# Optimization experiments

Measured on AMD Instinct MI355X. Metric: run time of the kernel, lower is better.

Reference implementation:

```python
import jax, jax.numpy as jnp
import numpy as np

N = 50000
IN_F = 200
OUT_F = 200
NRELA = 200
E1 = 400000
E2 = 100000
ALPHA = 0.2  # leakyrelu slope


def setup_inputs() -> dict:
    key = jax.random.key(0)
    ks = jax.random.split(key, 9)
    xav = float(np.sqrt(2.0 / (OUT_F + 2 * IN_F + NRELA))) * 1.414
    return {
        "x": jax.random.normal(ks[0], (N, IN_F), dtype=jnp.float32),
        "edge": jax.random.randint(ks[1], (2, E1), 0, N, dtype=jnp.int32),
        "edge_embed": jax.random.normal(ks[2], (E1, NRELA), dtype=jnp.float32),
        "edge_list_nhop": jax.random.randint(ks[3], (2, E2), 0, N, dtype=jnp.int32),
        "edge_embed_nhop": jax.random.normal(ks[4], (E2, NRELA), dtype=jnp.float32),
        "a": jax.random.normal(ks[5], (OUT_F, 2 * IN_F + NRELA), dtype=jnp.float32) * xav,
        "a_2": jax.random.normal(ks[6], (1, OUT_F), dtype=jnp.float32) * float(np.sqrt(2.0 / (1 + OUT_F))) * 1.414,
        "mlp_w": jax.random.normal(ks[7], (1, OUT_F), dtype=jnp.float32) * float(np.sqrt(1.0 / OUT_F)),
        "mlp_b": jnp.zeros((1,), dtype=jnp.float32),
    }


def reference(x, edge, edge_embed, edge_list_nhop, edge_embed_nhop, a, a_2, mlp_w, mlp_b):
    # concat 1-hop and n-hop edges: e [2,E], emb [E,nrela]
    e = jnp.concatenate([edge, edge_list_nhop], axis=1)
    emb = jnp.concatenate([edge_embed, edge_embed_nhop], axis=0)
    src = e[0]
    dst = e[1]
    n_edges = emb.shape[0]
    # edge_h: [E, 2*in + nrela]
    edge_h = jnp.concatenate([x[src], x[dst], emb], axis=1)
    # edge_m = a @ edge_h.T, kept as [E, out]
    edge_m = edge_h @ a.T
    # powers = -leakyrelu(a_2 @ edge_m): [E]
    powers = -jax.nn.leaky_relu(edge_m @ a_2[0], ALPHA)
    # inline MLP: tanh(Linear(edge_m)) -> [E]
    y = jnp.tanh(edge_m @ mlp_w[0] + mlp_b[0])
    powers = powers * y / n_edges
    edge_e = jnp.exp(powers)  # [E]
    n = x.shape[0]
    # segment-sum over source nodes (sparse.sum over dim=1 of coo[src,dst,:])
    e_rowsum = jax.ops.segment_sum(edge_e, src, num_segments=n)[:, None]  # [N,1]
    e_rowsum = jnp.where(e_rowsum == 0.0, 1e-12, e_rowsum)
    # weighted scatter-add of edge messages
    edge_w = edge_e[:, None] * edge_m  # [E, out]
    h_prime = jax.ops.segment_sum(edge_w, src, num_segments=n)  # [N, out]
    h_prime = h_prime / e_rowsum
    return jax.nn.elu(h_prime)  # concat=True
```

## Files before the change

### kernel.cpp

```cpp
#include <hip/hip_runtime.h>
#include <math.h>

#define NN    50000
#define FDIM  200
#define E1N   400000
#define E2N   100000
#define EN    500000

typedef __attribute__((ext_vector_type(8))) short short8;
typedef __attribute__((ext_vector_type(4))) float f32x4;

#define VALL_OFF   0
#define WALL_OFF   608
#define SCAL_OFF   1216
#define RS_OFF     201216
#define CNT_OFF    251216
#define FILL_OFF   301216
#define INCL_OFF   351216
#define BSUM_OFF   401216
#define SORT_OFF   401472
#define XB_OFF     1401472
#define AB_OFF     6401472
#define TSB_OFF    6461472

static __device__ __forceinline__ unsigned short f2bf(float f) {
    unsigned int u = __float_as_uint(f);
    unsigned int r = (u + 0x7fffu + ((u >> 16) & 1u)) >> 16;
    return (unsigned short)r;
}
static __device__ __forceinline__ float bf2f(unsigned short s) {
    return __uint_as_float((unsigned int)s << 16);
}

#define DPP_ADD(x, ctrl, rmask) \
    x += __int_as_float(__builtin_amdgcn_update_dpp(0, __float_as_int(x), ctrl, rmask, 0xf, true))

static __device__ __forceinline__ float wave_sum_bcast(float x) {
    DPP_ADD(x, 0x111, 0xf);
    DPP_ADD(x, 0x112, 0xf);
    DPP_ADD(x, 0x114, 0xf);
    DPP_ADD(x, 0x118, 0xf);
    DPP_ADD(x, 0x142, 0xa);
    DPP_ADD(x, 0x143, 0xc);
    return __int_as_float(__builtin_amdgcn_readlane(__float_as_int(x), 63));
}

__global__ void k_coeffs(const float* __restrict__ a, const float* __restrict__ a2,
                         const float* __restrict__ mlpw,
                         float* __restrict__ vall, float* __restrict__ wall) {
    int k = blockIdx.x * blockDim.x + threadIdx.x;
    if (k >= 600) return;
    float v = 0.f, w = 0.f;
    for (int o = 0; o < FDIM; ++o) {
        float av = a[o * 600 + k];
        v += a2[o] * av;
        w += mlpw[o] * av;
    }
    vall[k] = v;
    wall[k] = w;
}

__global__ __launch_bounds__(256) void k_node_scal(const float* __restrict__ x,
                                                   const float* __restrict__ vall,
                                                   const float* __restrict__ wall,
                                                   float* __restrict__ scal,
                                                   unsigned short* __restrict__ xb) {
    __shared__ float sv[1200];
    int tid = threadIdx.x;
    for (int i = tid; i < 1200; i += 256) sv[i] = (i < 600) ? vall[i] : wall[i - 600];
    __syncthreads();
    int lane = tid & 63;
    int n = blockIdx.x * 4 + (tid >> 6);
    float ps = 0.f, pd = 0.f, qs = 0.f, qd = 0.f;
    if (lane < 50) {
        float4 xv = *(const float4*)(x + (size_t)n * FDIM + lane * 4);
        float4 v1 = *(const float4*)(sv + lane * 4);
        float4 v2 = *(const float4*)(sv + 200 + lane * 4);
        float4 w1 = *(const float4*)(sv + 600 + lane * 4);
        float4 w2 = *(const float4*)(sv + 800 + lane * 4);
        ps = xv.x * v1.x + xv.y * v1.y + xv.z * v1.z + xv.w * v1.w;
        pd = xv.x * v2.x + xv.y * v2.y + xv.z * v2.z + xv.w * v2.w;
        qs = xv.x * w1.x + xv.y * w1.y + xv.z * w1.z + xv.w * w1.w;
        qd = xv.x * w2.x + xv.y * w2.y + xv.z * w2.z + xv.w * w2.w;
        ushort4 o;
        o.x = f2bf(xv.x); o.y = f2bf(xv.y); o.z = f2bf(xv.z); o.w = f2bf(xv.w);
        *(ushort4*)(xb + (size_t)n * FDIM + lane * 4) = o;
    }
    ps = wave_sum_bcast(ps);
    pd = wave_sum_bcast(pd);
    qs = wave_sum_bcast(qs);
    qd = wave_sum_bcast(qd);
    if (lane == 0) {
        float4 r = make_float4(ps, pd, qs, qd);
        *(float4*)(scal + (size_t)n * 4) = r;
    }
}

__global__ __launch_bounds__(256) void k_cvt(const float* __restrict__ src,
                                             unsigned short* __restrict__ dst, int n4) {
    int i = blockIdx.x * 256 + threadIdx.x;
    if (i >= n4) return;
    float4 v = *(const float4*)(src + (size_t)i * 4);
    ushort4 o;
    o.x = f2bf(v.x); o.y = f2bf(v.y); o.z = f2bf(v.z); o.w = f2bf(v.w);
    *(ushort4*)(dst + (size_t)i * 4) = o;
}

__global__ __launch_bounds__(256) void k_hist(const int* __restrict__ edge,
                                              const int* __restrict__ edgenh,
                                              int* __restrict__ counts) {
    int g = blockIdx.x * 256 + threadIdx.x;
    if (g >= EN) return;
    int s = (g < E1N) ? edge[g] : edgenh[g - E1N];
    atomicAdd(counts + s, 1);
}

__global__ __launch_bounds__(256) void k_scan1(const int* __restrict__ counts,
                                               int* __restrict__ incl,
                                               int* __restrict__ bsums) {
    __shared__ int tmp[256];
    int g = blockIdx.x * 256 + threadIdx.x;
    int v = (g < NN) ? counts[g] : 0;
    tmp[threadIdx.x] = v;
    __syncthreads();
    for (int off = 1; off < 256; off <<= 1) {
        int t = (threadIdx.x >= off) ? tmp[threadIdx.x - off] : 0;
        __syncthreads();
        tmp[threadIdx.x] += t;
        __syncthreads();
    }
    if (g < NN) incl[g] = tmp[threadIdx.x];
    if (threadIdx.x == 255) bsums[blockIdx.x] = tmp[255];
}

__global__ __launch_bounds__(256) void k_scan2(int* __restrict__ bsums, int nb) {
    __shared__ int tmp[256];
    int v = (threadIdx.x < nb) ? bsums[threadIdx.x] : 0;
    tmp[threadIdx.x] = v;
    __syncthreads();
    for (int off = 1; off < 256; off <<= 1) {
        int t = (threadIdx.x >= off) ? tmp[threadIdx.x - off] : 0;
        __syncthreads();
        tmp[threadIdx.x] += t;
        __syncthreads();
    }
    if (threadIdx.x < nb) bsums[threadIdx.x] = tmp[threadIdx.x] - v;
}

__global__ __launch_bounds__(256) void k_scan3(const int* __restrict__ counts,
                                               int* __restrict__ incl,
                                               const int* __restrict__ bsums,
                                               int* __restrict__ fill) {
    int g = blockIdx.x * 256 + threadIdx.x;
    if (g >= NN) return;
    int v = incl[g] - counts[g] + bsums[blockIdx.x];
    incl[g] = v;
    fill[g] = v;
}

__global__ __launch_bounds__(256) void k_scatter(const int* __restrict__ edge,
                                                 const int* __restrict__ edgenh,
                                                 int* __restrict__ fill,
                                                 int2* __restrict__ sorted2) {
    int g = blockIdx.x * 256 + threadIdx.x;
    if (g >= EN) return;
    int s, d;
    if (g < E1N) { s = edge[g]; d = edge[E1N + g]; }
    else { s = edgenh[g - E1N]; d = edgenh[E2N + (g - E1N)]; }
    int pos = atomicAdd(fill + s, 1);
    sorted2[pos] = make_int2(g, d);
}

__global__ __launch_bounds__(256) void k_csr(const int2* __restrict__ sorted2,
                                             const int* __restrict__ offs,
                                             const int* __restrict__ counts,
                                             const float* __restrict__ ee,
                                             const float* __restrict__ eenh,
                                             const unsigned short* __restrict__ xb,
                                             const float* __restrict__ vall,
                                             const float* __restrict__ wall,
                                             const float* __restrict__ scal,
                                             const float* __restrict__ mlpb,
                                             float* __restrict__ rowsum,
                                             unsigned short* __restrict__ Tsb) {
    int tid = threadIdx.x, lane = tid & 63;
    int n = blockIdx.x * 4 + (tid >> 6);
    float4 v3 = make_float4(0, 0, 0, 0), w3 = v3;
    if (lane < 50) {
        v3 = *(const float4*)(vall + 400 + lane * 4);
        w3 = *(const float4*)(wall + 400 + lane * 4);
    }
    float4 sc_n = *(const float4*)(scal + (size_t)n * 4);
    float mb = mlpb[0];
    int beg = offs[n], cnt = counts[n];
    float accx0 = 0, accx1 = 0, accx2 = 0, accx3 = 0;
    float acce0 = 0, acce1 = 0, acce2 = 0, acce3 = 0;
    float rs = 0.f;
    int2 ed = (cnt > 0) ? sorted2[beg] : make_int2(0, 0);
    float4 evc = make_float4(0, 0, 0, 0), xvc = evc;
    if (cnt > 0 && lane < 50) {
        const float* er = (ed.x < E1N) ? ee + (size_t)ed.x * FDIM
                                       : eenh + (size_t)(ed.x - E1N) * FDIM;
        evc = *(const float4*)(er + lane * 4);
        ushort4 xu = *(const ushort4*)(xb + (size_t)ed.y * FDIM + lane * 4);
        xvc.x = bf2f(xu.x); xvc.y = bf2f(xu.y); xvc.z = bf2f(xu.z); xvc.w = bf2f(xu.w);
    }
    for (int i = 0; i < cnt; ++i) {
        int2 edn = (i + 1 < cnt) ? sorted2[beg + i + 1] : ed;
        float4 evn = make_float4(0, 0, 0, 0), xvn = evn;
        if (i + 1 < cnt && lane < 50) {
            const float* ern = (edn.x < E1N) ? ee + (size_t)edn.x * FDIM
                                             : eenh + (size_t)(edn.x - E1N) * FDIM;
            evn = *(const float4*)(ern + lane * 4);
            ushort4 xu = *(const ushort4*)(xb + (size_t)edn.y * FDIM + lane * 4);
            xvn.x = bf2f(xu.x); xvn.y = bf2f(xu.y); xvn.z = bf2f(xu.z); xvn.w = bf2f(xu.w);
        }
        float pe = evc.x * v3.x + evc.y * v3.y + evc.z * v3.z + evc.w * v3.w;
        float qe = evc.x * w3.x + evc.y * w3.y + evc.z * w3.z + evc.w * w3.w;
        pe = wave_sum_bcast(pe);
        qe = wave_sum_bcast(qe);
        float4 sd = *(const float4*)(scal + (size_t)ed.y * 4);
        float z1 = sc_n.x + sd.y + pe;
        float z2 = sc_n.z + sd.w + qe + mb;
        float l = z1 > 0.f ? z1 : 0.2f * z1;
        float e2 = __expf(2.f * z2);
        float t = 1.f - 2.f * __builtin_amdgcn_rcpf(e2 + 1.f);
        float wgt = __expf(l * t * (-1.f / (float)EN));
        rs += wgt;
        accx0 += wgt * xvc.x; accx1 += wgt * xvc.y; accx2 += wgt * xvc.z; accx3 += wgt * xvc.w;
        acce0 += wgt * evc.x; acce1 += wgt * evc.y; acce2 += wgt * evc.z; acce3 += wgt * evc.w;
        ed = edn; evc = evn; xvc = xvn;
    }
    if (lane == 0) rowsum[n] = rs;
    float inv = (cnt > 0) ? __builtin_amdgcn_rcpf(rs) : 0.f;
    if (lane < 50) {
        ushort4 o1, o2;
        o1.x = f2bf(accx0 * inv); o1.y = f2bf(accx1 * inv);
        o1.z = f2bf(accx2 * inv); o1.w = f2bf(accx3 * inv);
        o2.x = f2bf(acce0 * inv); o2.y = f2bf(acce1 * inv);
        o2.z = f2bf(acce2 * inv); o2.w = f2bf(acce3 * inv);
        *(ushort4*)(Tsb + (size_t)n * 400 + lane * 4) = o1;
        *(ushort4*)(Tsb + (size_t)n * 400 + 200 + lane * 4) = o2;
    }
}

__global__ __launch_bounds__(256) void k_gemm_fused(const unsigned short* __restrict__ xb,
                                                    const unsigned short* __restrict__ tsb,
                                                    const unsigned short* __restrict__ ab,
                                                    const float* __restrict__ rowsum,
                                                    float* __restrict__ out) {
    __shared__ unsigned short Al[64][40];
    __shared__ unsigned short Bl[64][40];
    int tid = threadIdx.x, w = tid >> 6, lane = tid & 63;
    int h = blockIdx.y * 4 + blockIdx.x;
    int g = (h & 7) * 391 + (h >> 3);
    int by = g >> 2, bx = g & 3;
    f32x4 acc[4] = {};
    int r = tid >> 2, c = tid & 3;
    int arow = by * 64 + r;
    int brow = bx * 64 + r;
    bool inA = arow < NN;
    bool inB = brow < 200;
    const unsigned short* aPx = xb + (size_t)arow * 200;
    const unsigned short* aPt = tsb + (size_t)arow * 400;
    const unsigned short* bP = ab + (size_t)brow * 600;
    for (int k0 = 0; k0 < 640; k0 += 32) {
        int gk = k0 + c * 8;
        uint4 av = make_uint4(0, 0, 0, 0), bv = av;
        if (gk < 200) {
            if (inA) av = *(const uint4*)(aPx + gk);
            if (inB) bv = *(const uint4*)(bP + gk);
        } else if (gk >= 224 && gk < 624) {
            if (inA) av = *(const uint4*)(aPt + (gk - 224));
            if (inB) bv = *(const uint4*)(bP + gk - 24);
        }
        *(uint4*)&Al[r][c * 8] = av;
        *(uint4*)&Bl[r][c * 8] = bv;
        __syncthreads();
        short8 af = *(short8*)&Al[w * 16 + (lane & 15)][(lane >> 4) * 8];
        #pragma unroll
        for (int ct = 0; ct < 4; ++ct) {
            short8 bf = *(short8*)&Bl[ct * 16 + (lane & 15)][(lane >> 4) * 8];
            acc[ct] = __builtin_amdgcn_mfma_f32_16x16x32_bf16(af, bf, acc[ct], 0, 0, 0);
        }
        __syncthreads();
    }
    #pragma unroll
    for (int ct = 0; ct < 4; ++ct) {
        #pragma unroll
        for (int rr = 0; rr < 4; ++rr) {
            int grow = by * 64 + w * 16 + (lane >> 4) * 4 + rr;
            int gcol = bx * 64 + ct * 16 + (lane & 15);
            if (grow < NN && gcol < 200) {
                float rsv = rowsum[grow];
                float hh = acc[ct][rr];
                float o = (rsv == 0.f) ? 0.f : (hh > 0.f ? hh : expm1f(hh));
                out[(size_t)grow * 200 + gcol] = o;
            }
        }
    }
}

extern "C" void kernel_launch(void* const* d_in, const int* in_sizes, int n_in,
                              void* d_out, int out_size, void* d_ws, size_t ws_size,
                              hipStream_t stream) {
    const float* x      = (const float*)d_in[0];
    const int*   edge   = (const int*)d_in[1];
    const float* ee     = (const float*)d_in[2];
    const int*   edgenh = (const int*)d_in[3];
    const float* eenh   = (const float*)d_in[4];
    const float* a      = (const float*)d_in[5];
    const float* a2     = (const float*)d_in[6];
    const float* mlpw   = (const float*)d_in[7];
    const float* mlpb   = (const float*)d_in[8];

    float* ws = (float*)d_ws;
    float* vall   = ws + VALL_OFF;
    float* wall   = ws + WALL_OFF;
    float* scal   = ws + SCAL_OFF;
    float* rowsum = ws + RS_OFF;
    int*   counts = (int*)(ws + CNT_OFF);
    int*   fill   = (int*)(ws + FILL_OFF);
    int*   incl   = (int*)(ws + INCL_OFF);
    int*   bsums  = (int*)(ws + BSUM_OFF);
    int2*  sorted2 = (int2*)(ws + SORT_OFF);
    unsigned short* xb  = (unsigned short*)(ws + XB_OFF);
    unsigned short* ab  = (unsigned short*)(ws + AB_OFF);
    unsigned short* tsb = (unsigned short*)(ws + TSB_OFF);

    hipMemsetAsync(counts, 0, (size_t)(2 * NN) * sizeof(int), stream);

    k_coeffs<<<3, 256, 0, stream>>>(a, a2, mlpw, vall, wall);
    k_node_scal<<<NN / 4, 256, 0, stream>>>(x, vall, wall, scal, xb);
    k_cvt<<<(200 * 600 / 4 + 255) / 256, 256, 0, stream>>>(a, ab, 200 * 600 / 4);

    k_hist<<<(EN + 255) / 256, 256, 0, stream>>>(edge, edgenh, counts);
    int nb = (NN + 255) / 256;
    k_scan1<<<nb, 256, 0, stream>>>(counts, incl, bsums);
    k_scan2<<<1, 256, 0, stream>>>(bsums, nb);
    k_scan3<<<nb, 256, 0, stream>>>(counts, incl, bsums, fill);
    k_scatter<<<(EN + 255) / 256, 256, 0, stream>>>(edge, edgenh, fill, sorted2);

    k_csr<<<NN / 4, 256, 0, stream>>>(sorted2, incl, counts, ee, eenh, xb,
                                      vall, wall, scal, mlpb, rowsum, tsb);

    dim3 gg(4, (NN + 63) / 64);
    k_gemm_fused<<<gg, 256, 0, stream>>>(xb, tsb, ab, rowsum, (float*)d_out);
}
```

Before: 727.6 us.

## Batch edge records per wave and prefetch four gathers ahead in CSR loop

The per-node edge loop now loads up to 64 edge records, plus the destination node's scalar terms, in one coalesced per-lane read and broadcasts them with readlane. This replaces the serial sorted2 and scal loads that sat on each iteration's critical path. Gathers of edge-embedding and x rows are kept four edges in flight with a rotating set of registers, instead of one edge ahead. The costs are higher register pressure, padding to a multiple of four with masked-out weights, and readlane of zeroed records, which issues gathers of row 0 for padded slots.

```diff
diff --git a/kernel.cpp b/kernel.cpp
--- a/kernel.cpp
+++ b/kernel.cpp
@@ -43,6 +43,10 @@
     DPP_ADD(x, 0x142, 0xa);
     DPP_ADD(x, 0x143, 0xc);
     return __int_as_float(__builtin_amdgcn_readlane(__float_as_int(x), 63));
+}
+
+static __device__ __forceinline__ float readlane_f(float v, int l) {
+    return __int_as_float(__builtin_amdgcn_readlane(__float_as_int(v), l));
 }
 
 __global__ void k_coeffs(const float* __restrict__ a, const float* __restrict__ a2,
@@ -171,6 +175,37 @@
     sorted2[pos] = make_int2(g, d);
 }
 
+#define ISSUE(EV, XU, IDX) do {                                                   \
+    int _e = __builtin_amdgcn_readlane(recx, (IDX));                              \
+    int _d = __builtin_amdgcn_readlane(recy, (IDX));                              \
+    const float* _er = (_e < E1N) ? ee + (size_t)_e * FDIM                        \
+                                  : eenh + (size_t)(_e - E1N) * FDIM;             \
+    if (lane < 50) {                                                              \
+        EV = *(const float4*)(_er + lane * 4);                                    \
+        XU = *(const ushort4*)(xb + (size_t)_d * FDIM + lane * 4);                \
+    }                                                                             \
+} while (0)
+
+#define CONSUME(EV, XU, IDX) do {                                                 \
+    float _pe = EV.x * v3.x + EV.y * v3.y + EV.z * v3.z + EV.w * v3.w;            \
+    float _qe = EV.x * w3.x + EV.y * w3.y + EV.z * w3.z + EV.w * w3.w;            \
+    _pe = wave_sum_bcast(_pe);                                                    \
+    _qe = wave_sum_bcast(_qe);                                                    \
+    float _sdy = readlane_f(sdy, (IDX));                                          \
+    float _sdw = readlane_f(sdw, (IDX));                                          \
+    float _z1 = scx + _sdy + _pe;                                                 \
+    float _z2 = scz + _sdw + _qe + mb;                                            \
+    float _l = _z1 > 0.f ? _z1 : 0.2f * _z1;                                      \
+    float _e2 = __expf(2.f * _z2);                                                \
+    float _t = 1.f - 2.f * __builtin_amdgcn_rcpf(_e2 + 1.f);                      \
+    float _w = __expf(_l * _t * (-1.f / (float)EN));                              \
+    _w = ((IDX) < m) ? _w : 0.f;                                                  \
+    rs += _w;                                                                     \
+    float _x0 = bf2f(XU.x), _x1 = bf2f(XU.y), _x2 = bf2f(XU.z), _x3 = bf2f(XU.w); \
+    accx0 += _w * _x0; accx1 += _w * _x1; accx2 += _w * _x2; accx3 += _w * _x3;   \
+    acce0 += _w * EV.x; acce1 += _w * EV.y; acce2 += _w * EV.z; acce3 += _w * EV.w; \
+} while (0)
+
 __global__ __launch_bounds__(256) void k_csr(const int2* __restrict__ sorted2,
                                              const int* __restrict__ offs,
                                              const int* __restrict__ counts,
@@ -190,47 +225,39 @@
         v3 = *(const float4*)(vall + 400 + lane * 4);
         w3 = *(const float4*)(wall + 400 + lane * 4);
     }
-    float4 sc_n = *(const float4*)(scal + (size_t)n * 4);
+    float scx = scal[(size_t)n * 4 + 0];
+    float scz = scal[(size_t)n * 4 + 2];
     float mb = mlpb[0];
     int beg = offs[n], cnt = counts[n];
     float accx0 = 0, accx1 = 0, accx2 = 0, accx3 = 0;
     float acce0 = 0, acce1 = 0, acce2 = 0, acce3 = 0;
     float rs = 0.f;
-    int2 ed = (cnt > 0) ? sorted2[beg] : make_int2(0, 0);
-    float4 evc = make_float4(0, 0, 0, 0), xvc = evc;
-    if (cnt > 0 && lane < 50) {
-        const float* er = (ed.x < E1N) ? ee + (size_t)ed.x * FDIM
-                                       : eenh + (size_t)(ed.x - E1N) * FDIM;
-        evc = *(const float4*)(er + lane * 4);
-        ushort4 xu = *(const ushort4*)(xb + (size_t)ed.y * FDIM + lane * 4);
-        xvc.x = bf2f(xu.x); xvc.y = bf2f(xu.y); xvc.z = bf2f(xu.z); xvc.w = bf2f(xu.w);
-    }
-    for (int i = 0; i < cnt; ++i) {
-        int2 edn = (i + 1 < cnt) ? sorted2[beg + i + 1] : ed;
-        float4 evn = make_float4(0, 0, 0, 0), xvn = evn;
-        if (i + 1 < cnt && lane < 50) {
-            const float* ern = (edn.x < E1N) ? ee + (size_t)edn.x * FDIM
-                                             : eenh + (size_t)(edn.x - E1N) * FDIM;
-            evn = *(const float4*)(ern + lane * 4);
-            ushort4 xu = *(const ushort4*)(xb + (size_t)edn.y * FDIM + lane * 4);
-            xvn.x = bf2f(xu.x); xvn.y = bf2f(xu.y); xvn.z = bf2f(xu.z); xvn.w = bf2f(xu.w);
-        }
-        float pe = evc.x * v3.x + evc.y * v3.y + evc.z * v3.z + evc.w * v3.w;
-        float qe = evc.x * w3.x + evc.y * w3.y + evc.z * w3.z + evc.w * w3.w;
-        pe = wave_sum_bcast(pe);
-        qe = wave_sum_bcast(qe);
-        float4 sd = *(const float4*)(scal + (size_t)ed.y * 4);
-        float z1 = sc_n.x + sd.y + pe;
-        float z2 = sc_n.z + sd.w + qe + mb;
-        float l = z1 > 0.f ? z1 : 0.2f * z1;
-        float e2 = __expf(2.f * z2);
-        float t = 1.f - 2.f * __builtin_amdgcn_rcpf(e2 + 1.f);
-        float wgt = __expf(l * t * (-1.f / (float)EN));
-        rs += wgt;
-        accx0 += wgt * xvc.x; accx1 += wgt * xvc.y; accx2 += wgt * xvc.z; accx3 += wgt * xvc.w;
-        acce0 += wgt * evc.x; acce1 += wgt * evc.y; acce2 += wgt * evc.z; acce3 += wgt * evc.w;
-        ed = edn; evc = evn; xvc = xvn;
-    }
+
+    for (int c0 = 0; c0 < cnt; c0 += 64) {
+        int m = cnt - c0; if (m > 64) m = 64;
+        int recx = 0, recy = 0;
+        float sdy = 0.f, sdw = 0.f;
+        if (lane < m) {
+            int2 rr = sorted2[beg + c0 + lane];
+            recx = rr.x; recy = rr.y;
+            sdy = scal[(size_t)rr.y * 4 + 1];
+            sdw = scal[(size_t)rr.y * 4 + 3];
+        }
+        int m4 = (m + 3) & ~3;
+        float4 ev0 = make_float4(0,0,0,0), ev1 = ev0, ev2 = ev0, ev3 = ev0;
+        ushort4 xu0 = {0,0,0,0}, xu1 = xu0, xu2 = xu0, xu3 = xu0;
+        ISSUE(ev0, xu0, 0);
+        ISSUE(ev1, xu1, 1);
+        ISSUE(ev2, xu2, 2);
+        ISSUE(ev3, xu3, 3);
+        for (int i = 0; i < m4; i += 4) {
+            CONSUME(ev0, xu0, i + 0); if (i + 4 < m4) ISSUE(ev0, xu0, i + 4);
+            CONSUME(ev1, xu1, i + 1); if (i + 5 < m4) ISSUE(ev1, xu1, i + 5);
+            CONSUME(ev2, xu2, i + 2); if (i + 6 < m4) ISSUE(ev2, xu2, i + 6);
+            CONSUME(ev3, xu3, i + 3); if (i + 7 < m4) ISSUE(ev3, xu3, i + 7);
+        }
+    }
+
     if (lane == 0) rowsum[n] = rs;
     float inv = (cnt > 0) ? __builtin_amdgcn_rcpf(rs) : 0.f;
     if (lane < 50) {
```

Result: faster. 683.1 us (-6.1%).
